# Optimization experiments

Hardware: AMD Instinct MI355X
Metric: run time of the kernel (lower is better)

Reference implementation:

```python
import jax, jax.numpy as jnp
import numpy as np

TEMPERATURE = 8.0  # sqrt(d_head=64), from init_kwargs
NEG_INF = -1e9


def setup_inputs() -> dict:
    key = jax.random.key(0)
    k1, k2, k3, k4 = jax.random.split(key, 4)
    B, H, N, D = 2, 16, 2048, 64
    q = jax.random.normal(k1, (B, H, N, D), dtype=jnp.float32)
    k = jax.random.normal(k2, (B, H, N, D), dtype=jnp.float32)
    v = jax.random.normal(k3, (B, H, N, D), dtype=jnp.float32)
    mask = jax.random.randint(k4, (B, 1, N), 0, 2, dtype=jnp.int32)
    return {"q": q, "k": k, "v": v, "mask": mask}


def reference(q, k, v, mask):
    # scores: [B,H,N,N]
    attn = jnp.einsum("bhqd,bhkd->bhqk", q / TEMPERATURE, k)
    # symmetric padding mask: masked if row OR col token is masked
    m = mask.astype(attn.dtype)            # [B,1,N]
    row = m[:, :, :, None]                 # [B,1,N,1]
    col = m[:, :, None, :]                 # [B,1,1,N]
    sym = 1.0 - (1.0 - row) * (1.0 - col)  # [B,1,N,N], broadcasts over H
    attn = jnp.where(sym == 1.0, NEG_INF, attn)
    attn = jax.nn.softmax(attn, axis=-1)
    output = jnp.einsum("bhqk,bhkd->bhqd", attn, v)
    return output, attn
```

## Files before the change

kernel.cpp:

```cpp
#include <hip/hip_runtime.h>

typedef _Float16 half8 __attribute__((ext_vector_type(8)));
typedef _Float16 half4v __attribute__((ext_vector_type(4)));
typedef float f32x4 __attribute__((ext_vector_type(4)));

#if __has_builtin(__builtin_amdgcn_exp2f)
#define EXP2F(x) __builtin_amdgcn_exp2f(x)
#else
#define EXP2F(x) exp2f(x)
#endif

__global__ __launch_bounds__(256, 2)
void attn_fused(const float* __restrict__ qg_, const float* __restrict__ kg_,
                const float* __restrict__ vg_, const int* __restrict__ mg_,
                float* __restrict__ outg_, float* __restrict__ attng_)
{
    constexpr int N = 2048, D = 64, TM = 128, BK = 128, NCH = 16;
    constexpr int QS = 72, KS = 72, VTS = 136, PS = 72;
    constexpr float INVN = 1.0f / 2048.0f;
    constexpr float QSCALE = 1.44269504088896340736f * 0.125f;

    __shared__ _Float16 Qs[TM * QS];
    __shared__ _Float16 Ksh[BK * KS];
    __shared__ _Float16 Vts[D * VTS];
    __shared__ _Float16 Ps[TM * PS];
    __shared__ unsigned char cm[N];

    const int tid  = threadIdx.x;
    const int wid  = tid >> 6;
    const int lane = tid & 63;
    const int quad = lane >> 4;
    const int l15  = lane & 15;

    const int bh = blockIdx.x & 31;
    const int qt = blockIdx.x >> 5;
    const int b  = bh >> 4;

    const float* qg = qg_ + ((size_t)bh * N + qt * TM) * D;
    const float* kg = kg_ + (size_t)bh * N * D;
    const float* vg = vg_ + (size_t)bh * N * D;
    const int*   mg = mg_ + (size_t)b * N;
    float* attng = attng_ + ((size_t)bh * N + (size_t)qt * TM) * N;
    float* outg  = outg_  + ((size_t)bh * N + qt * TM) * D;

#pragma unroll
    for (int i = 0; i < 8; ++i) {
        int f = tid + 256 * i;
        int row = f >> 4, d = (f & 15) * 4;
        float4 x = *reinterpret_cast<const float4*>(qg + (size_t)row * D + d);
        half4v hv;
        hv[0] = (_Float16)(x.x * QSCALE);
        hv[1] = (_Float16)(x.y * QSCALE);
        hv[2] = (_Float16)(x.z * QSCALE);
        hv[3] = (_Float16)(x.w * QSCALE);
        *reinterpret_cast<half4v*>(&Qs[row * QS + d]) = hv;
        cm[f] = (unsigned char)(mg[f] ? 0 : 1);
    }

    float rowm[2][4];
#pragma unroll
    for (int mb = 0; mb < 2; ++mb)
#pragma unroll
        for (int r = 0; r < 4; ++r) {
            int row = qt * TM + wid * 32 + mb * 16 + quad * 4 + r;
            rowm[mb][r] = (float)mg[row];
        }

    __syncthreads();

    half8 qf[2][2];
#pragma unroll
    for (int mb = 0; mb < 2; ++mb)
#pragma unroll
        for (int ks = 0; ks < 2; ++ks)
            qf[mb][ks] = *reinterpret_cast<half8*>(
                &Qs[(wid * 32 + mb * 16 + l15) * QS + ks * 32 + quad * 8]);

    float lsum[2][4] = {{0,0,0,0},{0,0,0,0}};

    for (int kc = 0; kc < NCH; ++kc) {
        __syncthreads();
#pragma unroll
        for (int i = 0; i < 8; ++i) {
            int f = tid + 256 * i;
            int row = f >> 4, d = (f & 15) * 4;
            float4 x = *reinterpret_cast<const float4*>(kg + (size_t)(kc * BK + row) * D + d);
            half4v hv;
            hv[0] = (_Float16)x.x; hv[1] = (_Float16)x.y;
            hv[2] = (_Float16)x.z; hv[3] = (_Float16)x.w;
            *reinterpret_cast<half4v*>(&Ksh[row * KS + d]) = hv;
        }
        __syncthreads();

#pragma unroll
        for (int mb = 0; mb < 2; ++mb) {
#pragma unroll
            for (int nb = 0; nb < 8; ++nb) {
                f32x4 acc = {0.f, 0.f, 0.f, 0.f};
#pragma unroll
                for (int ks = 0; ks < 2; ++ks) {
                    half8 bf = *reinterpret_cast<half8*>(
                        &Ksh[(nb * 16 + l15) * KS + ks * 32 + quad * 8]);
                    acc = __builtin_amdgcn_mfma_f32_16x16x32_f16(qf[mb][ks], bf, acc, 0, 0, 0);
                }
                float cmf = (float)cm[kc * BK + nb * 16 + l15];
#pragma unroll
                for (int r = 0; r < 4; ++r)
                    lsum[mb][r] += cmf * EXP2F(acc[r]);
            }
        }
    }

#pragma unroll
    for (int mb = 0; mb < 2; ++mb)
#pragma unroll
        for (int r = 0; r < 4; ++r) {
            float s = lsum[mb][r];
            s += __shfl_xor(s, 1, 64);
            s += __shfl_xor(s, 2, 64);
            s += __shfl_xor(s, 4, 64);
            s += __shfl_xor(s, 8, 64);
            lsum[mb][r] = s;
        }

    float rscale[2][4], radd[2][4];
#pragma unroll
    for (int mb = 0; mb < 2; ++mb)
#pragma unroll
        for (int r = 0; r < 4; ++r) {
            bool uni = (rowm[mb][r] != 0.0f) || !(lsum[mb][r] > 0.0f);
            rscale[mb][r] = uni ? 0.0f : 1.0f / lsum[mb][r];
            radd[mb][r]   = uni ? INVN : 0.0f;
        }

    f32x4 Oacc[2][4];
#pragma unroll
    for (int mb = 0; mb < 2; ++mb)
#pragma unroll
        for (int nd = 0; nd < 4; ++nd)
            Oacc[mb][nd] = (f32x4){0.f, 0.f, 0.f, 0.f};

    for (int kc = 0; kc < NCH; ++kc) {
        __syncthreads();
#pragma unroll
        for (int i = 0; i < 8; ++i) {
            int f = tid + 256 * i;
            int row = f >> 4, d = (f & 15) * 4;
            float4 x = *reinterpret_cast<const float4*>(kg + (size_t)(kc * BK + row) * D + d);
            half4v hv;
            hv[0] = (_Float16)x.x; hv[1] = (_Float16)x.y;
            hv[2] = (_Float16)x.z; hv[3] = (_Float16)x.w;
            *reinterpret_cast<half4v*>(&Ksh[row * KS + d]) = hv;
        }
#pragma unroll
        for (int rr = 0; rr < 4; ++rr) {
            int key0 = rr * 32 + wid * 8;
            half8 hh;
#pragma unroll
            for (int j = 0; j < 8; ++j)
                hh[j] = (_Float16)vg[(size_t)(kc * BK + key0 + j) * D + lane];
            *reinterpret_cast<half8*>(&Vts[lane * VTS + key0]) = hh;
        }
        __syncthreads();

        f32x4 S[2][8];
#pragma unroll
        for (int mb = 0; mb < 2; ++mb)
#pragma unroll
            for (int nb = 0; nb < 8; ++nb) {
                f32x4 acc = {0.f, 0.f, 0.f, 0.f};
#pragma unroll
                for (int ks = 0; ks < 2; ++ks) {
                    half8 bf = *reinterpret_cast<half8*>(
                        &Ksh[(nb * 16 + l15) * KS + ks * 32 + quad * 8]);
                    acc = __builtin_amdgcn_mfma_f32_16x16x32_f16(qf[mb][ks], bf, acc, 0, 0, 0);
                }
                S[mb][nb] = acc;
            }

#pragma unroll
        for (int h = 0; h < 2; ++h) {
#pragma unroll
            for (int nb2 = 0; nb2 < 4; ++nb2) {
                int nb = h * 4 + nb2;
                float cmf = (float)cm[kc * BK + nb * 16 + l15];
#pragma unroll
                for (int mb = 0; mb < 2; ++mb) {
#pragma unroll
                    for (int r = 0; r < 4; ++r) {
                        float p = cmf * EXP2F(S[mb][nb][r]) * rscale[mb][r] + radd[mb][r];
                        Ps[(wid * 32 + mb * 16 + quad * 4 + r) * PS + nb2 * 16 + l15] = (_Float16)p;
                    }
                }
            }
            asm volatile("s_waitcnt lgkmcnt(0)" ::: "memory");

#pragma unroll
            for (int r8 = 0; r8 < 8; ++r8) {
                int rl = r8 * 4 + quad;
                half4v ph = *reinterpret_cast<half4v*>(
                    &Ps[(wid * 32 + rl) * PS + l15 * 4]);
                f32x4 pf;
                pf[0] = (float)ph[0]; pf[1] = (float)ph[1];
                pf[2] = (float)ph[2]; pf[3] = (float)ph[3];
                float* dst = attng + (size_t)(wid * 32 + rl) * N + kc * BK + h * 64 + l15 * 4;
                __builtin_nontemporal_store(pf, reinterpret_cast<f32x4*>(dst));
            }

#pragma unroll
            for (int ks = 0; ks < 2; ++ks) {
                half8 af[2];
#pragma unroll
                for (int mb = 0; mb < 2; ++mb)
                    af[mb] = *reinterpret_cast<half8*>(
                        &Ps[(wid * 32 + mb * 16 + l15) * PS + ks * 32 + quad * 8]);
#pragma unroll
                for (int nd = 0; nd < 4; ++nd) {
                    half8 bf = *reinterpret_cast<half8*>(
                        &Vts[(nd * 16 + l15) * VTS + h * 64 + ks * 32 + quad * 8]);
#pragma unroll
                    for (int mb = 0; mb < 2; ++mb)
                        Oacc[mb][nd] = __builtin_amdgcn_mfma_f32_16x16x32_f16(af[mb], bf, Oacc[mb][nd], 0, 0, 0);
                }
            }
        }
    }

#pragma unroll
    for (int mb = 0; mb < 2; ++mb)
#pragma unroll
        for (int nd = 0; nd < 4; ++nd)
#pragma unroll
            for (int r = 0; r < 4; ++r)
                __builtin_nontemporal_store(
                    Oacc[mb][nd][r],
                    outg + (size_t)(wid * 32 + mb * 16 + quad * 4 + r) * D + nd * 16 + l15);
}

extern "C" void kernel_launch(void* const* d_in, const int* in_sizes, int n_in,
                              void* d_out, int out_size, void* d_ws, size_t ws_size,
                              hipStream_t stream) {
    const float* q   = (const float*)d_in[0];
    const float* k   = (const float*)d_in[1];
    const float* v   = (const float*)d_in[2];
    const int*   msk = (const int*)d_in[3];
    float* out  = (float*)d_out;
    float* attn = out + (size_t)2 * 16 * 2048 * 64;
    dim3 grid(512), block(256);
    hipLaunchKernelGGL(attn_fused, grid, block, 0, stream, q, k, v, msk, out, attn);
}
```

Measured before the change: 650.0 us.

## Split attention into fp16 KV prep, row-sum, and main kernels with async LDS loads

Adds a prep kernel that converts K and V once to fp16 in swizzled, pre-transposed tiles in workspace. The row-sum and main passes then stream these tiles with global_load_lds double buffering and use 32x32x16 MFMA. The main pass builds the PV operand in registers via permlane32 swaps instead of an LDS round trip. The mask becomes an additive bias folded into the accumulator init. The goal is to stop re-converting fp32 K/V in every block and to overlap tile loads with compute. The cost is extra workspace traffic and two more launches, and the original fused kernel is kept as a fallback when workspace is insufficient.

Measured after the change: 1.239 ms. +90.6%, slower.

```diff
diff --git a/kernel.cpp b/kernel.cpp
--- a/kernel.cpp
+++ b/kernel.cpp
@@ -2,13 +2,300 @@
 
 typedef _Float16 half8 __attribute__((ext_vector_type(8)));
 typedef _Float16 half4v __attribute__((ext_vector_type(4)));
+typedef _Float16 half2v __attribute__((ext_vector_type(2)));
 typedef float f32x4 __attribute__((ext_vector_type(4)));
+typedef float f32x16 __attribute__((ext_vector_type(16)));
+typedef unsigned int u32;
+typedef u32 u32x4 __attribute__((ext_vector_type(4)));
+typedef int i32x4 __attribute__((ext_vector_type(4)));
 
 #if __has_builtin(__builtin_amdgcn_exp2f)
 #define EXP2F(x) __builtin_amdgcn_exp2f(x)
 #else
 #define EXP2F(x) exp2f(x)
 #endif
+
+#define QSCALE (1.44269504088896340736f * 0.125f)
+#define NEGBIG (-16384.0f)
+
+
+__device__ __forceinline__ void gload_lds16(const void* g, void* l) {
+    __builtin_amdgcn_global_load_lds(
+        (const __attribute__((address_space(1))) u32*)g,
+        (__attribute__((address_space(3))) u32*)l, 16, 0, 0);
+}
+
+__device__ __forceinline__ void stage_tile16k(const _Float16* g, _Float16* l,
+                                              int wid, int lane) {
+#pragma unroll
+    for (int i = 0; i < 4; ++i) {
+        const int base = (wid * 4 + i) * 1024;
+        gload_lds16((const char*)g + base + lane * 16, (char*)l + base);
+    }
+}
+
+__device__ __forceinline__ u32 pkh(float a, float b) {
+    half2v h; h[0] = (_Float16)a; h[1] = (_Float16)b;
+    return __builtin_bit_cast(u32, h);
+}
+
+__device__ __forceinline__ void swap32(u32 &a, u32 &b) {
+    asm volatile("v_permlane32_swap_b32 %0, %1" : "+v"(a), "+v"(b));
+}
+
+__global__ __launch_bounds__(256, 2)
+void prep_kv(const float* __restrict__ kg_, const float* __restrict__ vg_,
+             _Float16* __restrict__ kws_, _Float16* __restrict__ vws_)
+{
+    __shared__ float tile[128 * 68];
+    const int tid = threadIdx.x;
+    const int bh  = blockIdx.x & 31;
+    const int kc  = blockIdx.x >> 5;
+    const float* kg = kg_ + ((size_t)bh * 2048 + kc * 128) * 64;
+    const float* vg = vg_ + ((size_t)bh * 2048 + kc * 128) * 64;
+    _Float16* kt = kws_ + ((size_t)bh * 16 + kc) * 8192;
+    _Float16* vt = vws_ + ((size_t)bh * 16 + kc) * 8192;
+
+#pragma unroll
+    for (int i = 0; i < 8; ++i) {
+        int f = tid + 256 * i;
+        int r = f >> 4, c4 = f & 15;
+        f32x4 x = *reinterpret_cast<const f32x4*>(kg + r * 64 + c4 * 4);
+        *reinterpret_cast<f32x4*>(&tile[r * 68 + c4 * 4]) = x;
+    }
+    __syncthreads();
+#pragma unroll
+    for (int i = 0; i < 4; ++i) {
+        int s16 = tid + 256 * i;
+        int r = s16 >> 3, u = s16 & 7;
+        int cb = (u * 16) ^ ((r & 7) << 4);
+        int d0 = cb >> 1;
+        f32x4 x0 = *reinterpret_cast<const f32x4*>(&tile[r * 68 + d0]);
+        f32x4 x1 = *reinterpret_cast<const f32x4*>(&tile[r * 68 + d0 + 4]);
+        half8 h;
+#pragma unroll
+        for (int j = 0; j < 4; ++j) { h[j] = (_Float16)x0[j]; h[4 + j] = (_Float16)x1[j]; }
+        __builtin_nontemporal_store(h, reinterpret_cast<half8*>(kt + s16 * 8));
+    }
+    __syncthreads();
+#pragma unroll
+    for (int i = 0; i < 8; ++i) {
+        int f = tid + 256 * i;
+        int r = f >> 4, c4 = f & 15;
+        f32x4 x = *reinterpret_cast<const f32x4*>(vg + r * 64 + c4 * 4);
+        *reinterpret_cast<f32x4*>(&tile[r * 68 + c4 * 4]) = x;
+    }
+    __syncthreads();
+#pragma unroll
+    for (int i = 0; i < 4; ++i) {
+        int s16 = tid + 256 * i;
+        int r = s16 >> 4, u = s16 & 15;
+        int cb = (u * 16) ^ ((r & 7) << 4);
+        int k0 = cb >> 1;
+        half8 h;
+#pragma unroll
+        for (int j = 0; j < 8; ++j) h[j] = (_Float16)tile[(k0 + j) * 68 + r];
+        __builtin_nontemporal_store(h, reinterpret_cast<half8*>(vt + s16 * 8));
+    }
+}
+
+__global__ __launch_bounds__(256, 2)
+void attn_sums(const float* __restrict__ qg_, const _Float16* __restrict__ kws_,
+               const int* __restrict__ mg_, float* __restrict__ rsums_)
+{
+    __shared__ _Float16 Kb[2][8192];
+    __shared__ float biasF[2048];
+    const int tid = threadIdx.x, wid = tid >> 6, lane = tid & 63;
+    const int l31 = lane & 31, hi = lane >> 5;
+    const int bh = blockIdx.x & 31, qt = blockIdx.x >> 5;
+    const int* mg = mg_ + (bh >> 4) * 2048;
+    const _Float16* ktiles = kws_ + (size_t)bh * 16 * 8192;
+
+    const float* qrow = qg_ + ((size_t)bh * 2048 + qt * 128 + wid * 32 + l31) * 64;
+    half8 qf[4];
+#pragma unroll
+    for (int ks = 0; ks < 4; ++ks) {
+        f32x4 x0 = *reinterpret_cast<const f32x4*>(qrow + ks * 16 + hi * 8);
+        f32x4 x1 = *reinterpret_cast<const f32x4*>(qrow + ks * 16 + hi * 8 + 4);
+#pragma unroll
+        for (int j = 0; j < 4; ++j) {
+            qf[ks][j]     = (_Float16)(x0[j] * QSCALE);
+            qf[ks][4 + j] = (_Float16)(x1[j] * QSCALE);
+        }
+    }
+#pragma unroll
+    for (int i = 0; i < 2; ++i) {
+        int j = (tid + 256 * i) * 4;
+        i32x4 m = *reinterpret_cast<const i32x4*>(mg + j);
+        f32x4 bv;
+        bv[0] = m[0] ? NEGBIG : 0.f; bv[1] = m[1] ? NEGBIG : 0.f;
+        bv[2] = m[2] ? NEGBIG : 0.f; bv[3] = m[3] ? NEGBIG : 0.f;
+        *reinterpret_cast<f32x4*>(&biasF[j]) = bv;
+    }
+    stage_tile16k(ktiles, Kb[0], wid, lane);
+    __syncthreads();
+
+    float lsum = 0.f;
+    _Float16 *cur = Kb[0], *nxt = Kb[1];
+    for (int kc = 0; kc < 16; ++kc) {
+        if (kc < 15) stage_tile16k(ktiles + (size_t)(kc + 1) * 8192, nxt, wid, lane);
+        asm volatile("" ::: "memory");
+#pragma unroll
+        for (int kb = 0; kb < 4; ++kb) {
+            f32x16 acc;
+#pragma unroll
+            for (int g = 0; g < 4; ++g) {
+                f32x4 bv = *reinterpret_cast<const f32x4*>(
+                    &biasF[kc * 128 + kb * 32 + g * 8 + hi * 4]);
+                acc[4*g+0] = bv[0]; acc[4*g+1] = bv[1];
+                acc[4*g+2] = bv[2]; acc[4*g+3] = bv[3];
+            }
+            const int row = kb * 32 + l31;
+            const char* rbase = (const char*)cur + row * 128;
+            const int swz = (row & 7) << 4;
+#pragma unroll
+            for (int ks = 0; ks < 4; ++ks) {
+                half8 kf = *reinterpret_cast<const half8*>(rbase + ((ks * 32 + hi * 16) ^ swz));
+                acc = __builtin_amdgcn_mfma_f32_32x32x16_f16(kf, qf[ks], acc, 0, 0, 0);
+            }
+#pragma unroll
+            for (int r = 0; r < 16; ++r) lsum += EXP2F(acc[r]);
+        }
+        __syncthreads();
+        _Float16* t = cur; cur = nxt; nxt = t;
+    }
+    lsum += __shfl_xor(lsum, 32, 64);
+    if (hi == 0)
+        rsums_[(size_t)bh * 2048 + qt * 128 + wid * 32 + l31] = lsum;
+}
+
+__global__ __launch_bounds__(256, 2)
+void attn_main(const float* __restrict__ qg_, const _Float16* __restrict__ kws_,
+               const _Float16* __restrict__ vws_, const int* __restrict__ mg_,
+               const float* __restrict__ rsums_,
+               float* __restrict__ outg_, float* __restrict__ attng_)
+{
+    __shared__ _Float16 Kb[2][8192];
+    __shared__ _Float16 Vb[2][8192];
+    __shared__ float biasF[2048];
+    const int tid = threadIdx.x, wid = tid >> 6, lane = tid & 63;
+    const int l31 = lane & 31, hi = lane >> 5;
+    const int bh = blockIdx.x & 31, qt = blockIdx.x >> 5;
+    const int* mg = mg_ + (bh >> 4) * 2048;
+    const _Float16* ktiles = kws_ + (size_t)bh * 16 * 8192;
+    const _Float16* vtiles = vws_ + (size_t)bh * 16 * 8192;
+    const int qrow_l = qt * 128 + wid * 32 + l31;
+
+    const float* qrow = qg_ + ((size_t)bh * 2048 + qrow_l) * 64;
+    half8 qf[4];
+#pragma unroll
+    for (int ks = 0; ks < 4; ++ks) {
+        f32x4 x0 = *reinterpret_cast<const f32x4*>(qrow + ks * 16 + hi * 8);
+        f32x4 x1 = *reinterpret_cast<const f32x4*>(qrow + ks * 16 + hi * 8 + 4);
+#pragma unroll
+        for (int j = 0; j < 4; ++j) {
+            qf[ks][j]     = (_Float16)(x0[j] * QSCALE);
+            qf[ks][4 + j] = (_Float16)(x1[j] * QSCALE);
+        }
+    }
+#pragma unroll
+    for (int i = 0; i < 2; ++i) {
+        int j = (tid + 256 * i) * 4;
+        i32x4 m = *reinterpret_cast<const i32x4*>(mg + j);
+        f32x4 bv;
+        bv[0] = m[0] ? NEGBIG : 0.f; bv[1] = m[1] ? NEGBIG : 0.f;
+        bv[2] = m[2] ? NEGBIG : 0.f; bv[3] = m[3] ? NEGBIG : 0.f;
+        *reinterpret_cast<f32x4*>(&biasF[j]) = bv;
+    }
+
+    const float rs = rsums_[(size_t)bh * 2048 + qrow_l];
+    const int   rm = mg[qrow_l];
+    const bool uni = (rm != 0) || !(rs > 0.f);
+    const float rscale = uni ? 0.f : 1.f / rs;
+    const float radd   = uni ? (1.0f / 2048.0f) : 0.f;
+
+    stage_tile16k(ktiles, Kb[0], wid, lane);
+    stage_tile16k(vtiles, Vb[0], wid, lane);
+    __syncthreads();
+
+    f32x16 Oacc0, Oacc1;
+#pragma unroll
+    for (int r = 0; r < 16; ++r) { Oacc0[r] = 0.f; Oacc1[r] = 0.f; }
+
+    float* attnrow = attng_ + ((size_t)bh * 2048 + qrow_l) * 2048;
+    _Float16 *curK = Kb[0], *nxtK = Kb[1], *curV = Vb[0], *nxtV = Vb[1];
+
+    for (int kc = 0; kc < 16; ++kc) {
+        if (kc < 15) {
+            stage_tile16k(ktiles + (size_t)(kc + 1) * 8192, nxtK, wid, lane);
+            stage_tile16k(vtiles + (size_t)(kc + 1) * 8192, nxtV, wid, lane);
+        }
+        asm volatile("" ::: "memory");
+#pragma unroll
+        for (int kb = 0; kb < 4; ++kb) {
+            f32x16 acc;
+#pragma unroll
+            for (int g = 0; g < 4; ++g) {
+                f32x4 bv = *reinterpret_cast<const f32x4*>(
+                    &biasF[kc * 128 + kb * 32 + g * 8 + hi * 4]);
+                acc[4*g+0] = bv[0]; acc[4*g+1] = bv[1];
+                acc[4*g+2] = bv[2]; acc[4*g+3] = bv[3];
+            }
+            const int row = kb * 32 + l31;
+            const char* rbase = (const char*)curK + row * 128;
+            const int swz = (row & 7) << 4;
+#pragma unroll
+            for (int ks = 0; ks < 4; ++ks) {
+                half8 kf = *reinterpret_cast<const half8*>(rbase + ((ks * 32 + hi * 16) ^ swz));
+                acc = __builtin_amdgcn_mfma_f32_32x32x16_f16(kf, qf[ks], acc, 0, 0, 0);
+            }
+            float p[16];
+#pragma unroll
+            for (int r = 0; r < 16; ++r) p[r] = EXP2F(acc[r]) * rscale + radd;
+#pragma unroll
+            for (int g = 0; g < 4; ++g) {
+                f32x4 v; v[0] = p[4*g]; v[1] = p[4*g+1]; v[2] = p[4*g+2]; v[3] = p[4*g+3];
+                __builtin_nontemporal_store(v, reinterpret_cast<f32x4*>(
+                    attnrow + kc * 128 + kb * 32 + g * 8 + hi * 4));
+            }
+#pragma unroll
+            for (int s = 0; s < 2; ++s) {
+                u32 cA = pkh(p[8*s + 0], p[8*s + 1]);
+                u32 dA = pkh(p[8*s + 2], p[8*s + 3]);
+                u32 cB = pkh(p[8*s + 4], p[8*s + 5]);
+                u32 dB = pkh(p[8*s + 6], p[8*s + 7]);
+                swap32(cA, cB);
+                swap32(dA, dB);
+                u32x4 wv; wv[0] = cA; wv[1] = dA; wv[2] = cB; wv[3] = dB;
+                half8 af = __builtin_bit_cast(half8, wv);
+#pragma unroll
+                for (int nd = 0; nd < 2; ++nd) {
+                    const int vrow = nd * 32 + l31;
+                    half8 bf = *reinterpret_cast<const half8*>(
+                        (const char*)curV + vrow * 256 +
+                        ((kb * 64 + s * 32 + hi * 16) ^ ((vrow & 7) << 4)));
+                    if (nd == 0) Oacc0 = __builtin_amdgcn_mfma_f32_32x32x16_f16(af, bf, Oacc0, 0, 0, 0);
+                    else         Oacc1 = __builtin_amdgcn_mfma_f32_32x32x16_f16(af, bf, Oacc1, 0, 0, 0);
+                }
+            }
+        }
+        if (kc < 15) {
+            asm volatile("s_waitcnt vmcnt(16) lgkmcnt(0)" ::: "memory");
+            __builtin_amdgcn_s_barrier();
+            _Float16* t;
+            t = curK; curK = nxtK; nxtK = t;
+            t = curV; curV = nxtV; nxtV = t;
+        }
+    }
+
+    float* outg = outg_ + ((size_t)bh * 2048 + qt * 128) * 64;
+#pragma unroll
+    for (int r = 0; r < 16; ++r) {
+        int q_l = wid * 32 + (r & 3) + 8 * (r >> 2) + 4 * hi;
+        __builtin_nontemporal_store(Oacc0[r], outg + (size_t)q_l * 64 + l31);
+        __builtin_nontemporal_store(Oacc1[r], outg + (size_t)q_l * 64 + 32 + l31);
+    }
+}
 
 __global__ __launch_bounds__(256, 2)
 void attn_fused(const float* __restrict__ qg_, const float* __restrict__ kg_,
@@ -18,7 +305,6 @@
     constexpr int N = 2048, D = 64, TM = 128, BK = 128, NCH = 16;
     constexpr int QS = 72, KS = 72, VTS = 136, PS = 72;
     constexpr float INVN = 1.0f / 2048.0f;
-    constexpr float QSCALE = 1.44269504088896340736f * 0.125f;
 
     __shared__ _Float16 Qs[TM * QS];
     __shared__ _Float16 Ksh[BK * KS];
@@ -68,12 +354,12 @@
 
     __syncthreads();
 
-    half8 qf[2][2];
+    half8 qfr[2][2];
 #pragma unroll
     for (int mb = 0; mb < 2; ++mb)
 #pragma unroll
         for (int ks = 0; ks < 2; ++ks)
-            qf[mb][ks] = *reinterpret_cast<half8*>(
+            qfr[mb][ks] = *reinterpret_cast<half8*>(
                 &Qs[(wid * 32 + mb * 16 + l15) * QS + ks * 32 + quad * 8]);
 
     float lsum[2][4] = {{0,0,0,0},{0,0,0,0}};
@@ -99,9 +385,9 @@
                 f32x4 acc = {0.f, 0.f, 0.f, 0.f};
 #pragma unroll
                 for (int ks = 0; ks < 2; ++ks) {
-                    half8 bf = *reinterpret_cast<half8*>(
+                    half8 bfr = *reinterpret_cast<half8*>(
                         &Ksh[(nb * 16 + l15) * KS + ks * 32 + quad * 8]);
-                    acc = __builtin_amdgcn_mfma_f32_16x16x32_f16(qf[mb][ks], bf, acc, 0, 0, 0);
+                    acc = __builtin_amdgcn_mfma_f32_16x16x32_f16(qfr[mb][ks], bfr, acc, 0, 0, 0);
                 }
                 float cmf = (float)cm[kc * BK + nb * 16 + l15];
 #pragma unroll
@@ -171,9 +457,9 @@
                 f32x4 acc = {0.f, 0.f, 0.f, 0.f};
 #pragma unroll
                 for (int ks = 0; ks < 2; ++ks) {
-                    half8 bf = *reinterpret_cast<half8*>(
+                    half8 bfr = *reinterpret_cast<half8*>(
                         &Ksh[(nb * 16 + l15) * KS + ks * 32 + quad * 8]);
-                    acc = __builtin_amdgcn_mfma_f32_16x16x32_f16(qf[mb][ks], bf, acc, 0, 0, 0);
+                    acc = __builtin_amdgcn_mfma_f32_16x16x32_f16(qfr[mb][ks], bfr, acc, 0, 0, 0);
                 }
                 S[mb][nb] = acc;
             }
@@ -216,11 +502,11 @@
                         &Ps[(wid * 32 + mb * 16 + l15) * PS + ks * 32 + quad * 8]);
 #pragma unroll
                 for (int nd = 0; nd < 4; ++nd) {
-                    half8 bf = *reinterpret_cast<half8*>(
+                    half8 bfr = *reinterpret_cast<half8*>(
                         &Vts[(nd * 16 + l15) * VTS + h * 64 + ks * 32 + quad * 8]);
 #pragma unroll
                     for (int mb = 0; mb < 2; ++mb)
-                        Oacc[mb][nd] = __builtin_amdgcn_mfma_f32_16x16x32_f16(af[mb], bf, Oacc[mb][nd], 0, 0, 0);
+                        Oacc[mb][nd] = __builtin_amdgcn_mfma_f32_16x16x32_f16(af[mb], bfr, Oacc[mb][nd], 0, 0, 0);
                 }
             }
         }
@@ -246,6 +532,20 @@
     const int*   msk = (const int*)d_in[3];
     float* out  = (float*)d_out;
     float* attn = out + (size_t)2 * 16 * 2048 * 64;
-    dim3 grid(512), block(256);
-    hipLaunchKernelGGL(attn_fused, grid, block, 0, stream, q, k, v, msk, out, attn);
-}
+
+    const size_t kv_halves = (size_t)32 * 2048 * 64;
+    const size_t need = kv_halves * 2 * sizeof(_Float16)
+                      + (size_t)32 * 2048 * sizeof(float);
+    if (d_ws != nullptr && ws_size >= need) {
+        _Float16* kws = (_Float16*)d_ws;
+        _Float16* vws = kws + kv_halves;
+        float* rsums  = (float*)(vws + kv_halves);
+        hipLaunchKernelGGL(prep_kv,   dim3(512), dim3(256), 0, stream, k, v, kws, vws);
+        hipLaunchKernelGGL(attn_sums, dim3(512), dim3(256), 0, stream, q, kws, msk, rsums);
+        hipLaunchKernelGGL(attn_main, dim3(512), dim3(256), 0, stream,
+                           q, kws, vws, msk, rsums, out, attn);
+    } else {
+        hipLaunchKernelGGL(attn_fused, dim3(512), dim3(256), 0, stream,
+                           q, k, v, msk, out, attn);
+    }
+}
```
